# Optimization experiments

Measured on AMD Instinct MI355X. Metric: run time of the kernel, lower is better.

## Reference

```python
import jax, jax.numpy as jnp
import numpy as np

NN_SIZE = 10  # matches init_kwargs nn_size


def _knn_idx(points, k):
    """points: (B,N,D). Returns (B,N,k) indices of k nearest neighbors, self excluded."""
    sq = jnp.sum(points * points, axis=-1)  # (B,N)
    # squared euclidean distances (B,N,N)
    d2 = sq[:, :, None] + sq[:, None, :] - 2.0 * jnp.einsum('bnd,bmd->bnm', points, points)
    _, idx = jax.lax.top_k(-d2, k + 1)  # smallest distances; first hit is self
    return idx[:, :, 1:]  # drop self -> (B,N,k)


def _uniform_laplacian(points, knn_idx):
    """points: (B,N,D); knn_idx: (B,N,K). lap = mean(neighbors) - point."""
    neigh = jax.vmap(lambda p, i: p[i])(points, knn_idx)  # (B,N,K,D) gather per batch
    return jnp.mean(neigh, axis=2) - points


def setup_inputs() -> dict:
    key = jax.random.key(0)
    k1, k2 = jax.random.split(key)
    B, N, D = 2, 8192, 3
    point1 = jax.random.normal(k1, (B, N, D), dtype=jnp.float32)
    point2 = jax.random.normal(k2, (B, N, D), dtype=jnp.float32)
    return {"point1": point1, "point2": point2}


def reference(point1, point2):
    knn_idx = _knn_idx(point1, NN_SIZE)          # connectivity from ref cloud
    lap1 = _uniform_laplacian(point1, knn_idx)   # (B,N,3)
    lap2 = _uniform_laplacian(point2, knn_idx)   # reuse knn_idx
    # metric = L1Loss (mean reduction); use_norm=False
    return jnp.mean(jnp.abs(lap1 - lap2))
```

## Files before the change

kernel.cpp:

```cpp
#include <hip/hip_runtime.h>
#include <math.h>


constexpr int NPTS  = 8192;
constexpr int NB    = 2;
constexpr int KNN   = 10;
constexpr int QPB   = 64;
constexpr int WPB   = 16;
constexpr int BLOCK = QPB * WPB;
constexpr int MASK13 = 0xFFFFE000;

constexpr int   G    = 32;
constexpr int   NC   = G * G * G;
constexpr float BMIN = -5.5f;
constexpr float BW   = 11.0f;
constexpr float H    = BW / G;
constexpr float INVH = (float)G / BW;

__device__ __forceinline__ void ins1(int l[KNN], int x) {
#pragma unroll
    for (int k = KNN - 1; k > 0; --k) l[k] = min(l[k], max(l[k - 1], x));
    l[0] = min(l[0], x);
}
__device__ __forceinline__ void ins2(int l[KNN], int a, int b) {
    const int b0 = min(a, b), b1 = max(a, b);
#pragma unroll
    for (int k = KNN - 1; k >= 2; --k)
        l[k] = min(l[k], min(max(l[k - 1], b0), max(l[k - 2], b1)));
    l[1] = min(l[1], min(max(l[0], b0), b1));
    l[0] = min(l[0], b0);
}
template<int S>
__device__ __forceinline__ void ins2s(int l[KNN], int a, int b) {
    const int b0 = min(a, b), b1 = max(a, b);
#pragma unroll
    for (int k = KNN - 1; k >= S + 2; --k)
        l[k] = min(l[k], min(max(l[k - 1], b0), max(l[k - 2], b1)));
    l[S + 1] = min(l[S + 1], min(max(l[S], b0), b1));
    l[S] = min(l[S], b0);
}
__device__ __forceinline__ void merge_sorted(int l[KNN], const int p[KNN]) {
    ins2s<0>(l, p[0], p[1]);
    ins2s<2>(l, p[2], p[3]);
    ins2s<4>(l, p[4], p[5]);
    ins2s<6>(l, p[6], p[7]);
    ins2s<8>(l, p[8], p[9]);
}

__global__ void pack_bin(const float* __restrict__ p1, float4* __restrict__ w,
                         int* __restrict__ hist, int* __restrict__ cellof,
                         float* __restrict__ out, int* __restrict__ nfail) {
    const int i = blockIdx.x * blockDim.x + threadIdx.x;
    if (i >= NB * NPTS) return;
    if (i == 0) { out[0] = 0.0f; nfail[0] = 0; }
    const float x = p1[3 * i], y = p1[3 * i + 1], z = p1[3 * i + 2];
    w[i] = make_float4(x, y, z, fmaf(x, x, fmaf(y, y, z * z)));
    const int cx = min(max((int)floorf((x - BMIN) * INVH), 0), G - 1);
    const int cy = min(max((int)floorf((y - BMIN) * INVH), 0), G - 1);
    const int cz = min(max((int)floorf((z - BMIN) * INVH), 0), G - 1);
    const int c = (cz << 10) | (cy << 5) | cx;
    cellof[i] = c;
    atomicAdd(&hist[(i >> 13) * NC + c], 1);
}

__global__ __launch_bounds__(1024)
void scan_cells(const int* __restrict__ hist, int* __restrict__ starts) {
    __shared__ int wsum[16];
    const int b = blockIdx.x, t = threadIdx.x;
    const int* hb = hist + b * NC;
    int* sb = starts + b * (NC + 1);
    const int c0 = t * 32;
    int loc[32]; int sum = 0;
#pragma unroll
    for (int j = 0; j < 32; ++j) { loc[j] = hb[c0 + j]; sum += loc[j]; }
    const int lane = t & 63, wvi = t >> 6;
    int incl = sum;
#pragma unroll
    for (int off = 1; off < 64; off <<= 1) {
        const int v = __shfl_up(incl, off);
        if (lane >= off) incl += v;
    }
    if (lane == 63) wsum[wvi] = incl;
    __syncthreads();
    if (t < 16) {
        const int v = wsum[t];
        int iv = v;
#pragma unroll
        for (int off = 1; off < 16; off <<= 1) {
            const int u = __shfl_up(iv, off);
            if (t >= off) iv += u;
        }
        wsum[t] = iv - v;
    }
    __syncthreads();
    int run = wsum[wvi] + incl - sum;
#pragma unroll
    for (int j = 0; j < 32; ++j) { sb[c0 + j] = run; run += loc[j]; }
    if (t == 1023) sb[NC] = run;
}

__global__ void scatter_all(const int* __restrict__ cellof,
                            const int* __restrict__ starts,
                            int* __restrict__ hist,
                            const float4* __restrict__ w,
                            const float* __restrict__ p2,
                            float4* __restrict__ wsorted,
                            float4* __restrict__ p2s) {
    const int i = blockIdx.x * blockDim.x + threadIdx.x;
    if (i >= NB * NPTS) return;
    const int b = i >> 13;
    const int c = cellof[i];
    const int old = atomicSub(&hist[b * NC + c], 1);
    const int pos = b * NPTS + starts[b * (NC + 1) + c] + old - 1;
    wsorted[pos] = w[i];
    p2s[pos] = make_float4(p2[3 * i], p2[3 * i + 1], p2[3 * i + 2], 0.0f);
}

template<int S>
__device__ __forceinline__ void scan_batched(const float4* __restrict__ W,
                                             const int* __restrict__ st,
                                             int cx, int cy, int cz,
                                             float m2x, float m2y, float m2z,
                                             float q2, int qpos, int wv,
                                             int l[KNN])
{
    constexpr int Wd = 2 * S + 1;
    constexpr int R  = Wd * Wd;
    const int IMAX = 0x7FFFFFFF;
    int J0[R], J1[R];
#pragma unroll
    for (int r = 0; r < R; ++r) {
        const int dy = r % Wd - S, dz = r / Wd - S;
        const int ay = cy + dy, az = cz + dz;
        const bool ok = ((unsigned)ay < G) && ((unsigned)az < G);
        const int cbase = (az << 10) | (ay << 5);
        const int lo = cbase + max(cx - S, 0);
        const int hi = cbase + min(cx + S, G - 1) + 1;
        J0[r] = ok ? st[lo] : 0;
        J1[r] = ok ? st[hi] : 0;
    }
#pragma unroll
    for (int r = 0; r < R; ++r) {
        const int j1 = J1[r];
        int j = J0[r] + wv;
        if (j < j1) {
            float4 c4 = W[j];
            while (true) {
                const int jn = j + WPB;
                const bool more = jn < j1;
                float4 nx;
                if (more) nx = W[jn];
                const float d2 = fmaf(m2x, c4.x,
                                 fmaf(m2y, c4.y,
                                 fmaf(m2z, c4.z, c4.w + q2)));
                int key = (__float_as_int(d2) & MASK13) | j;
                key = (j == qpos) ? IMAX : key;
                ins1(l, key);
                if (!more) break;
                c4 = nx; j = jn;
            }
        }
    }
}

__global__ __launch_bounds__(BLOCK)
void phase1(const float4* __restrict__ wsorted, const float4* __restrict__ p2s,
            const int* __restrict__ starts, float* __restrict__ out,
            int* __restrict__ nfail, int* __restrict__ worklist)
{
    __shared__ int mv[WPB * KNN * QPB];

    const int batch = blockIdx.x >> 7;
    const int lane  = threadIdx.x & 63;
    const int wv    = __builtin_amdgcn_readfirstlane(threadIdx.x >> 6);
    const int qpos  = ((blockIdx.x & 127) << 6) + lane;

    const float4* W  = wsorted + batch * NPTS;
    const float4* P2 = p2s + batch * NPTS;
    const int*    st = starts + batch * (NC + 1);

    const float4 qp = W[qpos];
    const int cx = min(max((int)floorf((qp.x - BMIN) * INVH), 0), G - 1);
    const int cy = min(max((int)floorf((qp.y - BMIN) * INVH), 0), G - 1);
    const int cz = min(max((int)floorf((qp.z - BMIN) * INVH), 0), G - 1);
    const float lox = BMIN + cx * H, loy = BMIN + cy * H, loz = BMIN + cz * H;
    const float df = fminf(fminf(fminf(qp.x - lox, lox + H - qp.x),
                                 fminf(qp.y - loy, loy + H - qp.y)),
                           fminf(qp.z - loz, loz + H - qp.z));
    const float m2x = -2.0f * qp.x, m2y = -2.0f * qp.y, m2z = -2.0f * qp.z;
    const float q2 = qp.w;
    const int IMAX = 0x7FFFFFFF;

    const int sCov = (q2 > 4.8f) ? 2 : 1;

    int l[KNN];
#pragma unroll
    for (int k = 0; k < KNN; ++k) l[k] = IMAX;

    if (sCov == 1)
        scan_batched<1>(W, st, cx, cy, cz, m2x, m2y, m2z, q2, qpos, wv, l);
    else
        scan_batched<2>(W, st, cx, cy, cz, m2x, m2y, m2z, q2, qpos, wv, l);

#pragma unroll
    for (int k = 0; k < KNN; ++k) mv[(wv * KNN + k) * QPB + lane] = l[k];
    __syncthreads();

    if (threadIdx.x < QPB) {
        int M[KNN];
#pragma unroll
        for (int k = 0; k < KNN; ++k) M[k] = IMAX;
#pragma unroll
        for (int e = 0; e < WPB; ++e) {
            int p[KNN];
#pragma unroll
            for (int k = 0; k < KNN; ++k) p[k] = mv[(e * KNN + k) * QPB + lane];
            merge_sorted(M, p);
        }

        const float tau = __int_as_float(M[KNN - 1] & MASK13);
        const float R = (float)sCov * H + df;
        const bool covered = (tau <= R * R * 0.996f);
        float v = 0.0f;
        if (covered) {
            float s1x = 0, s1y = 0, s1z = 0, s2x = 0, s2y = 0, s2z = 0;
#pragma unroll
            for (int k = 0; k < KNN; ++k) {
                const int j = M[k] & (NPTS - 1);
                const float4 c4 = W[j];
                const float4 n2 = P2[j];
                s1x += c4.x; s1y += c4.y; s1z += c4.z;
                s2x += n2.x; s2y += n2.y; s2z += n2.z;
            }
            const float4 p2v = P2[qpos];
            const float dx = (s1x * 0.1f - qp.x) - (s2x * 0.1f - p2v.x);
            const float dy2 = (s1y * 0.1f - qp.y) - (s2y * 0.1f - p2v.y);
            const float dz2 = (s1z * 0.1f - qp.z) - (s2z * 0.1f - p2v.z);
            v = fabsf(dx) + fabsf(dy2) + fabsf(dz2);
        } else {
            const int wi = atomicAdd(nfail, 1);
            worklist[wi] = (batch << 16) | qpos;
        }
#pragma unroll
        for (int off = 32; off >= 1; off >>= 1) v += __shfl_down(v, off);
        if (threadIdx.x == 0)
            atomicAdd(out, v * (1.0f / (float)(NB * NPTS * 3)));
    }
}

constexpr int P2BLK = 256;
constexpr int P2GRID = 512;

__global__ __launch_bounds__(P2BLK)
void phase2(const float4* __restrict__ wsorted, const float4* __restrict__ p2s,
            const int* __restrict__ nfail, const int* __restrict__ worklist,
            float* __restrict__ out)
{
    const int lane = threadIdx.x & 63;
    const int wv   = threadIdx.x >> 6;
    const int wid  = blockIdx.x * (P2BLK / 64) + wv;
    const int NW   = P2GRID * (P2BLK / 64);
    const int nf   = *nfail;
    const int IMAX = 0x7FFFFFFF;
    float acc = 0.0f;

    for (int i = wid; i < nf; i += NW) {
        const int e = worklist[i];
        const int batch = e >> 16, qpos = e & 0xFFFF;
        const float4* W  = wsorted + batch * NPTS;
        const float4* P2 = p2s + batch * NPTS;
        const float4 qp = W[qpos];
        const float m2x = -2.0f * qp.x, m2y = -2.0f * qp.y, m2z = -2.0f * qp.z;
        const float q2 = qp.w;

        int l[KNN];
#pragma unroll
        for (int k = 0; k < KNN; ++k) l[k] = IMAX;

#pragma unroll 2
        for (int it = 0; it < NPTS / 128; ++it) {
            const int ja = it * 128 + lane, jb = ja + 64;
            const float4 ca = W[ja];
            const float4 cb = W[jb];
            const float da = fmaf(m2x, ca.x, fmaf(m2y, ca.y, fmaf(m2z, ca.z, ca.w + q2)));
            const float db = fmaf(m2x, cb.x, fmaf(m2y, cb.y, fmaf(m2z, cb.z, cb.w + q2)));
            int ka = (__float_as_int(da) & MASK13) | ja;
            int kb = (__float_as_int(db) & MASK13) | jb;
            ka = (ja == qpos) ? IMAX : ka;
            kb = (jb == qpos) ? IMAX : kb;
            ins2(l, ka, kb);
        }
        for (int off = 1; off < 64; off <<= 1) {
            int p[KNN];
#pragma unroll
            for (int k = 0; k < KNN; ++k) p[k] = __shfl_xor(l[k], off);
            merge_sorted(l, p);
        }
        float s1x = 0, s1y = 0, s1z = 0, s2x = 0, s2y = 0, s2z = 0;
#pragma unroll
        for (int k = 0; k < KNN; ++k) {
            const int j = l[k] & (NPTS - 1);
            const float4 c4 = W[j];
            const float4 n2 = P2[j];
            s1x += c4.x; s1y += c4.y; s1z += c4.z;
            s2x += n2.x; s2y += n2.y; s2z += n2.z;
        }
        const float4 p2v = P2[qpos];
        const float dx = (s1x * 0.1f - qp.x) - (s2x * 0.1f - p2v.x);
        const float dy = (s1y * 0.1f - qp.y) - (s2y * 0.1f - p2v.y);
        const float dz = (s1z * 0.1f - qp.z) - (s2z * 0.1f - p2v.z);
        if (lane == 0) acc += fabsf(dx) + fabsf(dy) + fabsf(dz);
    }

    if (lane == 0 && acc != 0.0f)
        atomicAdd(out, acc * (1.0f / (float)(NB * NPTS * 3)));
}

constexpr int FB_WPB = 8;
constexpr int FB_BLOCK = QPB * FB_WPB;
constexpr int CHUNK = NPTS / FB_WPB;

__global__ void prep_pack(const float* __restrict__ p, float4* __restrict__ w) {
    const int i = blockIdx.x * blockDim.x + threadIdx.x;
    if (i < NB * NPTS) {
        const float x = p[3 * i], y = p[3 * i + 1], z = p[3 * i + 2];
        w[i] = make_float4(x, y, z, fmaf(x, x, fmaf(y, y, z * z)));
    }
}

__global__ __launch_bounds__(FB_BLOCK, 2)
void knn_lap(const float4* __restrict__ w1, const float* __restrict__ p2,
             float* __restrict__ out)
{
    __shared__ int mv[FB_WPB * KNN * QPB];
    const int batch = blockIdx.x >> 7;
    const int qbase = (blockIdx.x & 127) << 6;
    const int lane  = threadIdx.x & 63;
    const int wv    = __builtin_amdgcn_readfirstlane(threadIdx.x >> 6);
    const int query = qbase + lane;
    const float4* Wb = w1 + batch * NPTS;
    const float4 qp = Wb[query];
    const float m2x = -2.0f * qp.x, m2y = -2.0f * qp.y, m2z = -2.0f * qp.z;
    const float q2 = qp.w;
    const int IMAX = 0x7FFFFFFF;
    int l[KNN];
#pragma unroll
    for (int k = 0; k < KNN; ++k) l[k] = IMAX;
    const int c0 = wv * CHUNK;
    const float4* cand = Wb + c0;
#pragma unroll 4
    for (int i = 0; i < CHUNK; i += 2) {
        const float4 ca = cand[i];
        const float4 cb = cand[i + 1];
        const int ja = c0 + i, jb = ja + 1;
        const float da = fmaf(m2x, ca.x, fmaf(m2y, ca.y, fmaf(m2z, ca.z, ca.w + q2)));
        const float db = fmaf(m2x, cb.x, fmaf(m2y, cb.y, fmaf(m2z, cb.z, cb.w + q2)));
        int ka = (__float_as_int(da) & MASK13) | ja;
        int kb = (__float_as_int(db) & MASK13) | jb;
        ka = (ja == query) ? IMAX : ka;
        kb = (jb == query) ? IMAX : kb;
        ins2(l, ka, kb);
    }
#pragma unroll
    for (int k = 0; k < KNN; ++k) mv[(wv * KNN + k) * QPB + lane] = l[k];
    __syncthreads();
    if (threadIdx.x < QPB) {
        int m[KNN];
#pragma unroll
        for (int k = 0; k < KNN; ++k) m[k] = IMAX;
#pragma unroll
        for (int e = 0; e < FB_WPB; ++e) {
            int p[KNN];
#pragma unroll
            for (int k = 0; k < KNN; ++k) p[k] = mv[(e * KNN + k) * QPB + lane];
            merge_sorted(m, p);
        }
        const float* P2b = p2 + (size_t)batch * NPTS * 3;
        float s1x = 0, s1y = 0, s1z = 0, s2x = 0, s2y = 0, s2z = 0;
#pragma unroll
        for (int k = 0; k < KNN; ++k) {
            const int j = m[k] & (NPTS - 1);
            const float4 c = Wb[j];
            s1x += c.x; s1y += c.y; s1z += c.z;
            s2x += P2b[3 * j + 0]; s2y += P2b[3 * j + 1]; s2z += P2b[3 * j + 2];
        }
        const int q = qbase + threadIdx.x;
        const float p2x = P2b[3 * q + 0], p2y = P2b[3 * q + 1], p2z = P2b[3 * q + 2];
        const float dx = (s1x * 0.1f - qp.x) - (s2x * 0.1f - p2x);
        const float dy = (s1y * 0.1f - qp.y) - (s2y * 0.1f - p2y);
        const float dz = (s1z * 0.1f - qp.z) - (s2z * 0.1f - p2z);
        float v = fabsf(dx) + fabsf(dy) + fabsf(dz);
#pragma unroll
        for (int off = 32; off >= 1; off >>= 1) v += __shfl_down(v, off);
        if (threadIdx.x == 0)
            atomicAdd(out, v * (1.0f / (float)(NB * NPTS * 3)));
    }
}

extern "C" void kernel_launch(void* const* d_in, const int* in_sizes, int n_in,
                              void* d_out, int out_size, void* d_ws, size_t ws_size,
                              hipStream_t stream) {
    const float* p1 = (const float*)d_in[0];
    const float* p2 = (const float*)d_in[1];
    float* out = (float*)d_out;

    size_t off = 0;
    float4* w       = (float4*)d_ws;               off += (size_t)NB * NPTS * 16;
    int*    hist    = (int*)((char*)d_ws + off);   off += (size_t)NB * NC * 4;
    int*    starts  = (int*)((char*)d_ws + off);   off += (size_t)NB * (NC + 1) * 4 + 8;
    int*    cellof  = (int*)((char*)d_ws + off);   off += (size_t)NB * NPTS * 4;
    float4* wsorted = (float4*)((char*)d_ws + off); off += (size_t)NB * NPTS * 16;
    float4* p2s     = (float4*)((char*)d_ws + off); off += (size_t)NB * NPTS * 16;
    int*    nfail   = (int*)((char*)d_ws + off);   off += 16;
    int*    worklist= (int*)((char*)d_ws + off);   off += (size_t)NB * NPTS * 4;

    if (ws_size < off) {
        hipMemsetAsync(out, 0, sizeof(float), stream);
        prep_pack<<<(NB * NPTS + 255) / 256, 256, 0, stream>>>(p1, w);
        knn_lap<<<NB * (NPTS / QPB), FB_BLOCK, 0, stream>>>(w, p2, out);
        return;
    }

    hipMemsetAsync(hist, 0, (size_t)NB * NC * 4, stream);
    pack_bin<<<(NB * NPTS + 255) / 256, 256, 0, stream>>>(p1, w, hist, cellof,
                                                          out, nfail);
    scan_cells<<<NB, 1024, 0, stream>>>(hist, starts);
    scatter_all<<<(NB * NPTS + 255) / 256, 256, 0, stream>>>(cellof, starts, hist,
                                                             w, p2, wsorted, p2s);
    phase1<<<NB * (NPTS / QPB), BLOCK, 0, stream>>>(wsorted, p2s, starts, out,
                                                    nfail, worklist);
    phase2<<<P2GRID, P2BLK, 0, stream>>>(wsorted, p2s, nfail, worklist, out);
}
```

Baseline: 120.9 us.

## Fuse binning, scan, scatter and kNN phases into one cooperative persistent kernel

Measured after the change: 265.9 us. +120.0%, slower.

```diff
diff --git a/kernel.cpp b/kernel.cpp
--- a/kernel.cpp
+++ b/kernel.cpp
@@ -1,13 +1,17 @@
 #include <hip/hip_runtime.h>
+#include <hip/hip_cooperative_groups.h>
 #include <math.h>
+
+namespace cg = cooperative_groups;
 
 
 constexpr int NPTS  = 8192;
 constexpr int NB    = 2;
 constexpr int KNN   = 10;
 constexpr int QPB   = 64;
-constexpr int WPB   = 16;
-constexpr int BLOCK = QPB * WPB;
+constexpr int WPB   = 8;
+constexpr int BLOCK = 512;
+constexpr int GRID  = 256;
 constexpr int MASK13 = 0xFFFFE000;
 
 constexpr int   G    = 32;
@@ -47,186 +51,257 @@
     ins2s<8>(l, p[8], p[9]);
 }
 
-__global__ void pack_bin(const float* __restrict__ p1, float4* __restrict__ w,
-                         int* __restrict__ hist, int* __restrict__ cellof,
-                         float* __restrict__ out, int* __restrict__ nfail) {
-    const int i = blockIdx.x * blockDim.x + threadIdx.x;
-    if (i >= NB * NPTS) return;
-    if (i == 0) { out[0] = 0.0f; nfail[0] = 0; }
-    const float x = p1[3 * i], y = p1[3 * i + 1], z = p1[3 * i + 2];
-    w[i] = make_float4(x, y, z, fmaf(x, x, fmaf(y, y, z * z)));
-    const int cx = min(max((int)floorf((x - BMIN) * INVH), 0), G - 1);
-    const int cy = min(max((int)floorf((y - BMIN) * INVH), 0), G - 1);
-    const int cz = min(max((int)floorf((z - BMIN) * INVH), 0), G - 1);
-    const int c = (cz << 10) | (cy << 5) | cx;
-    cellof[i] = c;
-    atomicAdd(&hist[(i >> 13) * NC + c], 1);
-}
-
-__global__ __launch_bounds__(1024)
-void scan_cells(const int* __restrict__ hist, int* __restrict__ starts) {
-    __shared__ int wsum[16];
-    const int b = blockIdx.x, t = threadIdx.x;
-    const int* hb = hist + b * NC;
-    int* sb = starts + b * (NC + 1);
-    const int c0 = t * 32;
-    int loc[32]; int sum = 0;
-#pragma unroll
-    for (int j = 0; j < 32; ++j) { loc[j] = hb[c0 + j]; sum += loc[j]; }
-    const int lane = t & 63, wvi = t >> 6;
-    int incl = sum;
+template<int S>
+__device__ __forceinline__ void scan_slab(const float4* __restrict__ W,
+                                          const int* __restrict__ st,
+                                          int cx, int cy, int cz,
+                                          float m2x, float m2y, float m2z,
+                                          float q2, int qpos, int wv,
+                                          int l[KNN])
+{
+    constexpr int Wd = 2 * S + 1;
+    const int IMAX = 0x7FFFFFFF;
+    const int xlo = max(cx - S, 0), xhi = min(cx + S, G - 1) + 1;
+#pragma unroll
+    for (int zi = 0; zi < Wd; ++zi) {
+        const int az = cz + zi - S;
+        int J0[Wd], J1[Wd];
+#pragma unroll
+        for (int yi = 0; yi < Wd; ++yi) {
+            const int ay = cy + yi - S;
+            const bool ok = ((unsigned)ay < G) && ((unsigned)az < G);
+            const int cbase = (az << 10) | (ay << 5);
+            J0[yi] = ok ? st[cbase + xlo] : 0;
+            J1[yi] = ok ? st[cbase + xhi] : 0;
+        }
+#pragma unroll
+        for (int yi = 0; yi < Wd; ++yi) {
+            const int j1 = J1[yi];
+            int j = J0[yi] + wv;
+            if (j < j1) {
+                float4 c4 = W[j];
+                while (true) {
+                    const int jn = j + WPB;
+                    const bool more = jn < j1;
+                    float4 nx;
+                    if (more) nx = W[jn];
+                    const float d2 = fmaf(m2x, c4.x,
+                                     fmaf(m2y, c4.y,
+                                     fmaf(m2z, c4.z, c4.w + q2)));
+                    int key = (__float_as_int(d2) & MASK13) | j;
+                    key = (j == qpos) ? IMAX : key;
+                    ins1(l, key);
+                    if (!more) break;
+                    c4 = nx; j = jn;
+                }
+            }
+        }
+    }
+}
+
+__global__ __launch_bounds__(BLOCK)
+void mega(const float* __restrict__ p1, const float* __restrict__ p2,
+          float* __restrict__ out,
+          float4* __restrict__ w, int* __restrict__ hist,
+          int* __restrict__ starts, int* __restrict__ cellof,
+          float4* __restrict__ wsorted, float4* __restrict__ p2s,
+          int* __restrict__ nfail, int* __restrict__ worklist,
+          int* __restrict__ blockTot)
+{
+    cg::grid_group grid = cg::this_grid();
+
+    __shared__ int mv[WPB * KNN * QPB];
+    __shared__ int wtot[8], wexcl[8], wred[8], sOff[1];
+
+    const int b    = blockIdx.x;
+    const int t    = threadIdx.x;
+    const int gtid = b * BLOCK + t;
+    const int lane = t & 63;
+    const int wv   = t >> 6;
+    const int IMAX = 0x7FFFFFFF;
+
+    if (gtid < NB * NC) hist[gtid] = 0;
+    if (gtid == 0) { out[0] = 0.0f; nfail[0] = 0; }
+    grid.sync();
+
+    if (gtid < NB * NPTS) {
+        const float x = p1[3 * gtid], y = p1[3 * gtid + 1], z = p1[3 * gtid + 2];
+        w[gtid] = make_float4(x, y, z, fmaf(x, x, fmaf(y, y, z * z)));
+        const int cx = min(max((int)floorf((x - BMIN) * INVH), 0), G - 1);
+        const int cy = min(max((int)floorf((y - BMIN) * INVH), 0), G - 1);
+        const int cz = min(max((int)floorf((z - BMIN) * INVH), 0), G - 1);
+        const int c = (cz << 10) | (cy << 5) | cx;
+        cellof[gtid] = c;
+        atomicAdd(&hist[(gtid >> 13) * NC + c], 1);
+    }
+    grid.sync();
+
+    const int batchC = b >> 7;
+    const int bb     = b & 127;
+    int cnt = (t < 256) ? hist[b * 256 + t] : 0;
+    int incl = cnt;
 #pragma unroll
     for (int off = 1; off < 64; off <<= 1) {
         const int v = __shfl_up(incl, off);
         if (lane >= off) incl += v;
     }
-    if (lane == 63) wsum[wvi] = incl;
+    if (lane == 63) wtot[wv] = incl;
     __syncthreads();
-    if (t < 16) {
-        const int v = wsum[t];
-        int iv = v;
-#pragma unroll
-        for (int off = 1; off < 16; off <<= 1) {
-            const int u = __shfl_up(iv, off);
-            if (t >= off) iv += u;
-        }
-        wsum[t] = iv - v;
+    if (t < 8) {
+        int o = 0;
+        for (int k = 0; k < t; ++k) o += wtot[k];
+        wexcl[t] = o;
     }
     __syncthreads();
-    int run = wsum[wvi] + incl - sum;
-#pragma unroll
-    for (int j = 0; j < 32; ++j) { sb[c0 + j] = run; run += loc[j]; }
-    if (t == 1023) sb[NC] = run;
-}
-
-__global__ void scatter_all(const int* __restrict__ cellof,
-                            const int* __restrict__ starts,
-                            int* __restrict__ hist,
-                            const float4* __restrict__ w,
-                            const float* __restrict__ p2,
-                            float4* __restrict__ wsorted,
-                            float4* __restrict__ p2s) {
-    const int i = blockIdx.x * blockDim.x + threadIdx.x;
-    if (i >= NB * NPTS) return;
-    const int b = i >> 13;
-    const int c = cellof[i];
-    const int old = atomicSub(&hist[b * NC + c], 1);
-    const int pos = b * NPTS + starts[b * (NC + 1) + c] + old - 1;
-    wsorted[pos] = w[i];
-    p2s[pos] = make_float4(p2[3 * i], p2[3 * i + 1], p2[3 * i + 2], 0.0f);
-}
-
-template<int S>
-__device__ __forceinline__ void scan_batched(const float4* __restrict__ W,
-                                             const int* __restrict__ st,
-                                             int cx, int cy, int cz,
-                                             float m2x, float m2y, float m2z,
-                                             float q2, int qpos, int wv,
-                                             int l[KNN])
-{
-    constexpr int Wd = 2 * S + 1;
-    constexpr int R  = Wd * Wd;
-    const int IMAX = 0x7FFFFFFF;
-    int J0[R], J1[R];
-#pragma unroll
-    for (int r = 0; r < R; ++r) {
-        const int dy = r % Wd - S, dz = r / Wd - S;
-        const int ay = cy + dy, az = cz + dz;
-        const bool ok = ((unsigned)ay < G) && ((unsigned)az < G);
-        const int cbase = (az << 10) | (ay << 5);
-        const int lo = cbase + max(cx - S, 0);
-        const int hi = cbase + min(cx + S, G - 1) + 1;
-        J0[r] = ok ? st[lo] : 0;
-        J1[r] = ok ? st[hi] : 0;
-    }
-#pragma unroll
-    for (int r = 0; r < R; ++r) {
-        const int j1 = J1[r];
-        int j = J0[r] + wv;
-        if (j < j1) {
-            float4 c4 = W[j];
-            while (true) {
-                const int jn = j + WPB;
-                const bool more = jn < j1;
-                float4 nx;
-                if (more) nx = W[jn];
-                const float d2 = fmaf(m2x, c4.x,
-                                 fmaf(m2y, c4.y,
-                                 fmaf(m2z, c4.z, c4.w + q2)));
-                int key = (__float_as_int(d2) & MASK13) | j;
-                key = (j == qpos) ? IMAX : key;
-                ins1(l, key);
-                if (!more) break;
-                c4 = nx; j = jn;
-            }
-        }
-    }
-}
-
-__global__ __launch_bounds__(BLOCK)
-void phase1(const float4* __restrict__ wsorted, const float4* __restrict__ p2s,
-            const int* __restrict__ starts, float* __restrict__ out,
-            int* __restrict__ nfail, int* __restrict__ worklist)
-{
-    __shared__ int mv[WPB * KNN * QPB];
-
-    const int batch = blockIdx.x >> 7;
-    const int lane  = threadIdx.x & 63;
-    const int wv    = __builtin_amdgcn_readfirstlane(threadIdx.x >> 6);
-    const int qpos  = ((blockIdx.x & 127) << 6) + lane;
-
-    const float4* W  = wsorted + batch * NPTS;
-    const float4* P2 = p2s + batch * NPTS;
-    const int*    st = starts + batch * (NC + 1);
-
-    const float4 qp = W[qpos];
-    const int cx = min(max((int)floorf((qp.x - BMIN) * INVH), 0), G - 1);
-    const int cy = min(max((int)floorf((qp.y - BMIN) * INVH), 0), G - 1);
-    const int cz = min(max((int)floorf((qp.z - BMIN) * INVH), 0), G - 1);
-    const float lox = BMIN + cx * H, loy = BMIN + cy * H, loz = BMIN + cz * H;
-    const float df = fminf(fminf(fminf(qp.x - lox, lox + H - qp.x),
-                                 fminf(qp.y - loy, loy + H - qp.y)),
-                           fminf(qp.z - loz, loz + H - qp.z));
-    const float m2x = -2.0f * qp.x, m2y = -2.0f * qp.y, m2z = -2.0f * qp.z;
-    const float q2 = qp.w;
-    const int IMAX = 0x7FFFFFFF;
-
-    const int sCov = (q2 > 4.8f) ? 2 : 1;
-
-    int l[KNN];
-#pragma unroll
-    for (int k = 0; k < KNN; ++k) l[k] = IMAX;
-
-    if (sCov == 1)
-        scan_batched<1>(W, st, cx, cy, cz, m2x, m2y, m2z, q2, qpos, wv, l);
-    else
-        scan_batched<2>(W, st, cx, cy, cz, m2x, m2y, m2z, q2, qpos, wv, l);
-
-#pragma unroll
-    for (int k = 0; k < KNN; ++k) mv[(wv * KNN + k) * QPB + lane] = l[k];
-    __syncthreads();
-
-    if (threadIdx.x < QPB) {
-        int M[KNN];
-#pragma unroll
-        for (int k = 0; k < KNN; ++k) M[k] = IMAX;
-#pragma unroll
-        for (int e = 0; e < WPB; ++e) {
-            int p[KNN];
-#pragma unroll
-            for (int k = 0; k < KNN; ++k) p[k] = mv[(e * KNN + k) * QPB + lane];
-            merge_sorted(M, p);
-        }
-
-        const float tau = __int_as_float(M[KNN - 1] & MASK13);
-        const float R = (float)sCov * H + df;
-        const bool covered = (tau <= R * R * 0.996f);
-        float v = 0.0f;
-        if (covered) {
+    const int excl = wexcl[wv] + incl - cnt;
+    if (t == 0) blockTot[b] = wexcl[7] + wtot[7];
+    if (t == 0 && bb == 0) starts[batchC * (NC + 1) + NC] = NPTS;
+    grid.sync();
+
+    {
+        const int base = batchC << 7;
+        int v = (t < bb) ? blockTot[base + t] : 0;
+#pragma unroll
+        for (int off = 32; off >= 1; off >>= 1) v += __shfl_xor(v, off);
+        if (lane == 0) wred[wv] = v;
+        __syncthreads();
+        if (t == 0) {
+            int o = 0;
+#pragma unroll
+            for (int k = 0; k < 8; ++k) o += wred[k];
+            sOff[0] = o;
+        }
+        __syncthreads();
+        if (t < 256)
+            starts[batchC * (NC + 1) + bb * 256 + t] = excl + sOff[0];
+    }
+    grid.sync();
+
+    if (gtid < NB * NPTS) {
+        const int bt = gtid >> 13;
+        const int c = cellof[gtid];
+        const int old = atomicSub(&hist[bt * NC + c], 1);
+        const int pos = bt * NPTS + starts[bt * (NC + 1) + c] + old - 1;
+        wsorted[pos] = w[gtid];
+        p2s[pos] = make_float4(p2[3 * gtid], p2[3 * gtid + 1],
+                               p2[3 * gtid + 2], 0.0f);
+    }
+    grid.sync();
+
+    {
+        const int batch = b >> 7;
+        const int qpos  = ((b & 127) << 6) + lane;
+        const float4* W  = wsorted + batch * NPTS;
+        const float4* P2 = p2s + batch * NPTS;
+        const int*    st = starts + batch * (NC + 1);
+
+        const float4 qp = W[qpos];
+        const int cx = min(max((int)floorf((qp.x - BMIN) * INVH), 0), G - 1);
+        const int cy = min(max((int)floorf((qp.y - BMIN) * INVH), 0), G - 1);
+        const int cz = min(max((int)floorf((qp.z - BMIN) * INVH), 0), G - 1);
+        const float lox = BMIN + cx * H, loy = BMIN + cy * H, loz = BMIN + cz * H;
+        const float df = fminf(fminf(fminf(qp.x - lox, lox + H - qp.x),
+                                     fminf(qp.y - loy, loy + H - qp.y)),
+                               fminf(qp.z - loz, loz + H - qp.z));
+        const float m2x = -2.0f * qp.x, m2y = -2.0f * qp.y, m2z = -2.0f * qp.z;
+        const float q2 = qp.w;
+        const int sCov = (q2 > 4.8f) ? 2 : 1;
+
+        int l[KNN];
+#pragma unroll
+        for (int k = 0; k < KNN; ++k) l[k] = IMAX;
+
+        if (sCov == 1)
+            scan_slab<1>(W, st, cx, cy, cz, m2x, m2y, m2z, q2, qpos, wv, l);
+        else
+            scan_slab<2>(W, st, cx, cy, cz, m2x, m2y, m2z, q2, qpos, wv, l);
+
+#pragma unroll
+        for (int k = 0; k < KNN; ++k) mv[(wv * KNN + k) * QPB + lane] = l[k];
+        __syncthreads();
+
+        if (t < QPB) {
+            int M[KNN];
+#pragma unroll
+            for (int k = 0; k < KNN; ++k) M[k] = IMAX;
+#pragma unroll
+            for (int e = 0; e < WPB; ++e) {
+                int p[KNN];
+#pragma unroll
+                for (int k = 0; k < KNN; ++k) p[k] = mv[(e * KNN + k) * QPB + lane];
+                merge_sorted(M, p);
+            }
+            const float tau = __int_as_float(M[KNN - 1] & MASK13);
+            const float R = (float)sCov * H + df;
+            const bool covered = (tau <= R * R * 0.996f);
+            float v = 0.0f;
+            if (covered) {
+                float s1x = 0, s1y = 0, s1z = 0, s2x = 0, s2y = 0, s2z = 0;
+#pragma unroll
+                for (int k = 0; k < KNN; ++k) {
+                    const int j = M[k] & (NPTS - 1);
+                    const float4 c4 = W[j];
+                    const float4 n2 = P2[j];
+                    s1x += c4.x; s1y += c4.y; s1z += c4.z;
+                    s2x += n2.x; s2y += n2.y; s2z += n2.z;
+                }
+                const float4 p2v = P2[qpos];
+                const float dx = (s1x * 0.1f - qp.x) - (s2x * 0.1f - p2v.x);
+                const float dy = (s1y * 0.1f - qp.y) - (s2y * 0.1f - p2v.y);
+                const float dz = (s1z * 0.1f - qp.z) - (s2z * 0.1f - p2v.z);
+                v = fabsf(dx) + fabsf(dy) + fabsf(dz);
+            } else {
+                const int wi = atomicAdd(nfail, 1);
+                worklist[wi] = (batch << 16) | qpos;
+            }
+#pragma unroll
+            for (int off = 32; off >= 1; off >>= 1) v += __shfl_down(v, off);
+            if (t == 0)
+                atomicAdd(out, v * (1.0f / (float)(NB * NPTS * 3)));
+        }
+    }
+    grid.sync();
+
+    {
+        const int nf = nfail[0];
+        const int wid = b * WPB + wv;
+        const int NW = GRID * WPB;
+        float acc = 0.0f;
+        for (int i = wid; i < nf; i += NW) {
+            const int e = worklist[i];
+            const int batch = e >> 16, qpos = e & 0xFFFF;
+            const float4* W  = wsorted + batch * NPTS;
+            const float4* P2 = p2s + batch * NPTS;
+            const float4 qp = W[qpos];
+            const float m2x = -2.0f * qp.x, m2y = -2.0f * qp.y, m2z = -2.0f * qp.z;
+            const float q2 = qp.w;
+
+            int l[KNN];
+#pragma unroll
+            for (int k = 0; k < KNN; ++k) l[k] = IMAX;
+#pragma unroll 2
+            for (int it = 0; it < NPTS / 128; ++it) {
+                const int ja = it * 128 + lane, jb = ja + 64;
+                const float4 ca = W[ja];
+                const float4 cb = W[jb];
+                const float da = fmaf(m2x, ca.x, fmaf(m2y, ca.y, fmaf(m2z, ca.z, ca.w + q2)));
+                const float db = fmaf(m2x, cb.x, fmaf(m2y, cb.y, fmaf(m2z, cb.z, cb.w + q2)));
+                int ka = (__float_as_int(da) & MASK13) | ja;
+                int kb = (__float_as_int(db) & MASK13) | jb;
+                ka = (ja == qpos) ? IMAX : ka;
+                kb = (jb == qpos) ? IMAX : kb;
+                ins2(l, ka, kb);
+            }
+            for (int off = 1; off < 64; off <<= 1) {
+                int p[KNN];
+#pragma unroll
+                for (int k = 0; k < KNN; ++k) p[k] = __shfl_xor(l[k], off);
+                merge_sorted(l, p);
+            }
             float s1x = 0, s1y = 0, s1z = 0, s2x = 0, s2y = 0, s2z = 0;
 #pragma unroll
             for (int k = 0; k < KNN; ++k) {
-                const int j = M[k] & (NPTS - 1);
+                const int j = l[k] & (NPTS - 1);
                 const float4 c4 = W[j];
                 const float4 n2 = P2[j];
                 s1x += c4.x; s1y += c4.y; s1z += c4.z;
@@ -234,86 +309,13 @@
             }
             const float4 p2v = P2[qpos];
             const float dx = (s1x * 0.1f - qp.x) - (s2x * 0.1f - p2v.x);
-            const float dy2 = (s1y * 0.1f - qp.y) - (s2y * 0.1f - p2v.y);
-            const float dz2 = (s1z * 0.1f - qp.z) - (s2z * 0.1f - p2v.z);
-            v = fabsf(dx) + fabsf(dy2) + fabsf(dz2);
-        } else {
-            const int wi = atomicAdd(nfail, 1);
-            worklist[wi] = (batch << 16) | qpos;
-        }
-#pragma unroll
-        for (int off = 32; off >= 1; off >>= 1) v += __shfl_down(v, off);
-        if (threadIdx.x == 0)
-            atomicAdd(out, v * (1.0f / (float)(NB * NPTS * 3)));
-    }
-}
-
-constexpr int P2BLK = 256;
-constexpr int P2GRID = 512;
-
-__global__ __launch_bounds__(P2BLK)
-void phase2(const float4* __restrict__ wsorted, const float4* __restrict__ p2s,
-            const int* __restrict__ nfail, const int* __restrict__ worklist,
-            float* __restrict__ out)
-{
-    const int lane = threadIdx.x & 63;
-    const int wv   = threadIdx.x >> 6;
-    const int wid  = blockIdx.x * (P2BLK / 64) + wv;
-    const int NW   = P2GRID * (P2BLK / 64);
-    const int nf   = *nfail;
-    const int IMAX = 0x7FFFFFFF;
-    float acc = 0.0f;
-
-    for (int i = wid; i < nf; i += NW) {
-        const int e = worklist[i];
-        const int batch = e >> 16, qpos = e & 0xFFFF;
-        const float4* W  = wsorted + batch * NPTS;
-        const float4* P2 = p2s + batch * NPTS;
-        const float4 qp = W[qpos];
-        const float m2x = -2.0f * qp.x, m2y = -2.0f * qp.y, m2z = -2.0f * qp.z;
-        const float q2 = qp.w;
-
-        int l[KNN];
-#pragma unroll
-        for (int k = 0; k < KNN; ++k) l[k] = IMAX;
-
-#pragma unroll 2
-        for (int it = 0; it < NPTS / 128; ++it) {
-            const int ja = it * 128 + lane, jb = ja + 64;
-            const float4 ca = W[ja];
-            const float4 cb = W[jb];
-            const float da = fmaf(m2x, ca.x, fmaf(m2y, ca.y, fmaf(m2z, ca.z, ca.w + q2)));
-            const float db = fmaf(m2x, cb.x, fmaf(m2y, cb.y, fmaf(m2z, cb.z, cb.w + q2)));
-            int ka = (__float_as_int(da) & MASK13) | ja;
-            int kb = (__float_as_int(db) & MASK13) | jb;
-            ka = (ja == qpos) ? IMAX : ka;
-            kb = (jb == qpos) ? IMAX : kb;
-            ins2(l, ka, kb);
-        }
-        for (int off = 1; off < 64; off <<= 1) {
-            int p[KNN];
-#pragma unroll
-            for (int k = 0; k < KNN; ++k) p[k] = __shfl_xor(l[k], off);
-            merge_sorted(l, p);
-        }
-        float s1x = 0, s1y = 0, s1z = 0, s2x = 0, s2y = 0, s2z = 0;
-#pragma unroll
-        for (int k = 0; k < KNN; ++k) {
-            const int j = l[k] & (NPTS - 1);
-            const float4 c4 = W[j];
-            const float4 n2 = P2[j];
-            s1x += c4.x; s1y += c4.y; s1z += c4.z;
-            s2x += n2.x; s2y += n2.y; s2z += n2.z;
-        }
-        const float4 p2v = P2[qpos];
-        const float dx = (s1x * 0.1f - qp.x) - (s2x * 0.1f - p2v.x);
-        const float dy = (s1y * 0.1f - qp.y) - (s2y * 0.1f - p2v.y);
-        const float dz = (s1z * 0.1f - qp.z) - (s2z * 0.1f - p2v.z);
-        if (lane == 0) acc += fabsf(dx) + fabsf(dy) + fabsf(dz);
-    }
-
-    if (lane == 0 && acc != 0.0f)
-        atomicAdd(out, acc * (1.0f / (float)(NB * NPTS * 3)));
+            const float dy = (s1y * 0.1f - qp.y) - (s2y * 0.1f - p2v.y);
+            const float dz = (s1z * 0.1f - qp.z) - (s2z * 0.1f - p2v.z);
+            if (lane == 0) acc += fabsf(dx) + fabsf(dy) + fabsf(dz);
+        }
+        if (lane == 0 && acc != 0.0f)
+            atomicAdd(out, acc * (1.0f / (float)(NB * NPTS * 3)));
+    }
 }
 
 constexpr int FB_WPB = 8;
@@ -405,14 +407,15 @@
     float* out = (float*)d_out;
 
     size_t off = 0;
-    float4* w       = (float4*)d_ws;               off += (size_t)NB * NPTS * 16;
-    int*    hist    = (int*)((char*)d_ws + off);   off += (size_t)NB * NC * 4;
-    int*    starts  = (int*)((char*)d_ws + off);   off += (size_t)NB * (NC + 1) * 4 + 8;
-    int*    cellof  = (int*)((char*)d_ws + off);   off += (size_t)NB * NPTS * 4;
+    float4* w       = (float4*)d_ws;                off += (size_t)NB * NPTS * 16;
+    int*    hist    = (int*)((char*)d_ws + off);    off += (size_t)NB * NC * 4;
+    int*    starts  = (int*)((char*)d_ws + off);    off += (size_t)NB * (NC + 1) * 4 + 8;
+    int*    cellof  = (int*)((char*)d_ws + off);    off += (size_t)NB * NPTS * 4;
     float4* wsorted = (float4*)((char*)d_ws + off); off += (size_t)NB * NPTS * 16;
     float4* p2s     = (float4*)((char*)d_ws + off); off += (size_t)NB * NPTS * 16;
-    int*    nfail   = (int*)((char*)d_ws + off);   off += 16;
-    int*    worklist= (int*)((char*)d_ws + off);   off += (size_t)NB * NPTS * 4;
+    int*    nfail   = (int*)((char*)d_ws + off);    off += 16;
+    int*    worklist= (int*)((char*)d_ws + off);    off += (size_t)NB * NPTS * 4;
+    int*    blockTot= (int*)((char*)d_ws + off);    off += (size_t)GRID * 4;
 
     if (ws_size < off) {
         hipMemsetAsync(out, 0, sizeof(float), stream);
@@ -421,13 +424,10 @@
         return;
     }
 
-    hipMemsetAsync(hist, 0, (size_t)NB * NC * 4, stream);
-    pack_bin<<<(NB * NPTS + 255) / 256, 256, 0, stream>>>(p1, w, hist, cellof,
-                                                          out, nfail);
-    scan_cells<<<NB, 1024, 0, stream>>>(hist, starts);
-    scatter_all<<<(NB * NPTS + 255) / 256, 256, 0, stream>>>(cellof, starts, hist,
-                                                             w, p2, wsorted, p2s);
-    phase1<<<NB * (NPTS / QPB), BLOCK, 0, stream>>>(wsorted, p2s, starts, out,
-                                                    nfail, worklist);
-    phase2<<<P2GRID, P2BLK, 0, stream>>>(wsorted, p2s, nfail, worklist, out);
-}
+    void* args[] = { (void*)&p1, (void*)&p2, (void*)&out, (void*)&w,
+                     (void*)&hist, (void*)&starts, (void*)&cellof,
+                     (void*)&wsorted, (void*)&p2s, (void*)&nfail,
+                     (void*)&worklist, (void*)&blockTot };
+    hipLaunchCooperativeKernel((void*)mega, dim3(GRID), dim3(BLOCK),
+                               args, 0, stream);
+}
```

## Fuse brute-force fallback into phase1 and gather p2 via sorted-index map

Applied to the files above, without the earlier changes.

Measured after the change: 147.7 us. +22.2%, slower.

```diff
diff --git a/kernel.cpp b/kernel.cpp
--- a/kernel.cpp
+++ b/kernel.cpp
@@ -6,7 +6,7 @@
 constexpr int NB    = 2;
 constexpr int KNN   = 10;
 constexpr int QPB   = 64;
-constexpr int WPB   = 16;
+constexpr int WPB   = 8;
 constexpr int BLOCK = QPB * WPB;
 constexpr int MASK13 = 0xFFFFE000;
 
@@ -49,10 +49,10 @@
 
 __global__ void pack_bin(const float* __restrict__ p1, float4* __restrict__ w,
                          int* __restrict__ hist, int* __restrict__ cellof,
-                         float* __restrict__ out, int* __restrict__ nfail) {
+                         float* __restrict__ out) {
     const int i = blockIdx.x * blockDim.x + threadIdx.x;
     if (i >= NB * NPTS) return;
-    if (i == 0) { out[0] = 0.0f; nfail[0] = 0; }
+    if (i == 0) out[0] = 0.0f;
     const float x = p1[3 * i], y = p1[3 * i + 1], z = p1[3 * i + 2];
     w[i] = make_float4(x, y, z, fmaf(x, x, fmaf(y, y, z * z)));
     const int cx = min(max((int)floorf((x - BMIN) * INVH), 0), G - 1);
@@ -103,9 +103,8 @@
                             const int* __restrict__ starts,
                             int* __restrict__ hist,
                             const float4* __restrict__ w,
-                            const float* __restrict__ p2,
                             float4* __restrict__ wsorted,
-                            float4* __restrict__ p2s) {
+                            int* __restrict__ sIdx) {
     const int i = blockIdx.x * blockDim.x + threadIdx.x;
     if (i >= NB * NPTS) return;
     const int b = i >> 13;
@@ -113,7 +112,7 @@
     const int old = atomicSub(&hist[b * NC + c], 1);
     const int pos = b * NPTS + starts[b * (NC + 1) + c] + old - 1;
     wsorted[pos] = w[i];
-    p2s[pos] = make_float4(p2[3 * i], p2[3 * i + 1], p2[3 * i + 2], 0.0f);
+    sIdx[pos] = i & (NPTS - 1);
 }
 
 template<int S>
@@ -164,20 +163,27 @@
 }
 
 __global__ __launch_bounds__(BLOCK)
-void phase1(const float4* __restrict__ wsorted, const float4* __restrict__ p2s,
-            const int* __restrict__ starts, float* __restrict__ out,
-            int* __restrict__ nfail, int* __restrict__ worklist)
+void phase1(const float4* __restrict__ wsorted, const int* __restrict__ sIdx,
+            const float* __restrict__ p2, const int* __restrict__ starts,
+            float* __restrict__ out)
 {
     __shared__ int mv[WPB * KNN * QPB];
+    __shared__ int failList[QPB];
+    __shared__ int nFail;
+    __shared__ float bsum;
 
     const int batch = blockIdx.x >> 7;
-    const int lane  = threadIdx.x & 63;
-    const int wv    = __builtin_amdgcn_readfirstlane(threadIdx.x >> 6);
+    const int t     = threadIdx.x;
+    const int lane  = t & 63;
+    const int wv    = __builtin_amdgcn_readfirstlane(t >> 6);
     const int qpos  = ((blockIdx.x & 127) << 6) + lane;
 
     const float4* W  = wsorted + batch * NPTS;
-    const float4* P2 = p2s + batch * NPTS;
+    const int*    sI = sIdx + batch * NPTS;
+    const float*  P2 = p2 + (size_t)batch * NPTS * 3;
     const int*    st = starts + batch * (NC + 1);
+
+    if (t == 0) { nFail = 0; bsum = 0.0f; }
 
     const float4 qp = W[qpos];
     const int cx = min(max((int)floorf((qp.x - BMIN) * INVH), 0), G - 1);
@@ -206,7 +212,7 @@
     for (int k = 0; k < KNN; ++k) mv[(wv * KNN + k) * QPB + lane] = l[k];
     __syncthreads();
 
-    if (threadIdx.x < QPB) {
+    if (t < QPB) {
         int M[KNN];
 #pragma unroll
         for (int k = 0; k < KNN; ++k) M[k] = IMAX;
@@ -228,97 +234,87 @@
             for (int k = 0; k < KNN; ++k) {
                 const int j = M[k] & (NPTS - 1);
                 const float4 c4 = W[j];
-                const float4 n2 = P2[j];
+                const int oi = sI[j];
                 s1x += c4.x; s1y += c4.y; s1z += c4.z;
-                s2x += n2.x; s2y += n2.y; s2z += n2.z;
+                s2x += P2[3 * oi + 0];
+                s2y += P2[3 * oi + 1];
+                s2z += P2[3 * oi + 2];
             }
-            const float4 p2v = P2[qpos];
-            const float dx = (s1x * 0.1f - qp.x) - (s2x * 0.1f - p2v.x);
-            const float dy2 = (s1y * 0.1f - qp.y) - (s2y * 0.1f - p2v.y);
-            const float dz2 = (s1z * 0.1f - qp.z) - (s2z * 0.1f - p2v.z);
-            v = fabsf(dx) + fabsf(dy2) + fabsf(dz2);
-        } else {
-            const int wi = atomicAdd(nfail, 1);
-            worklist[wi] = (batch << 16) | qpos;
-        }
+            const int oq = sI[qpos];
+            const float p2x = P2[3 * oq + 0];
+            const float p2y = P2[3 * oq + 1];
+            const float p2z = P2[3 * oq + 2];
+            const float dx = (s1x * 0.1f - qp.x) - (s2x * 0.1f - p2x);
+            const float dy = (s1y * 0.1f - qp.y) - (s2y * 0.1f - p2y);
+            const float dz = (s1z * 0.1f - qp.z) - (s2z * 0.1f - p2z);
+            v = fabsf(dx) + fabsf(dy) + fabsf(dz);
+        }
+        const unsigned long long fm = __ballot(!covered);
+        if (!covered) {
+            const int rank = __popcll(fm & ((1ull << lane) - 1ull));
+            failList[rank] = lane;
+        }
+        if (lane == 0) nFail = __popcll(fm);
 #pragma unroll
         for (int off = 32; off >= 1; off >>= 1) v += __shfl_down(v, off);
-        if (threadIdx.x == 0)
-            atomicAdd(out, v * (1.0f / (float)(NB * NPTS * 3)));
-    }
-}
-
-constexpr int P2BLK = 256;
-constexpr int P2GRID = 512;
-
-__global__ __launch_bounds__(P2BLK)
-void phase2(const float4* __restrict__ wsorted, const float4* __restrict__ p2s,
-            const int* __restrict__ nfail, const int* __restrict__ worklist,
-            float* __restrict__ out)
-{
-    const int lane = threadIdx.x & 63;
-    const int wv   = threadIdx.x >> 6;
-    const int wid  = blockIdx.x * (P2BLK / 64) + wv;
-    const int NW   = P2GRID * (P2BLK / 64);
-    const int nf   = *nfail;
-    const int IMAX = 0x7FFFFFFF;
+        if (lane == 0) bsum = v;
+    }
+    __syncthreads();
+
+    const int nf = nFail;
     float acc = 0.0f;
-
-    for (int i = wid; i < nf; i += NW) {
-        const int e = worklist[i];
-        const int batch = e >> 16, qpos = e & 0xFFFF;
-        const float4* W  = wsorted + batch * NPTS;
-        const float4* P2 = p2s + batch * NPTS;
-        const float4 qp = W[qpos];
-        const float m2x = -2.0f * qp.x, m2y = -2.0f * qp.y, m2z = -2.0f * qp.z;
-        const float q2 = qp.w;
-
-        int l[KNN];
-#pragma unroll
-        for (int k = 0; k < KNN; ++k) l[k] = IMAX;
-
+    for (int i = wv; i < nf; i += WPB) {
+        const int fq = ((blockIdx.x & 127) << 6) + failList[i];
+        const float4 fqp = W[fq];
+        const float f2x = -2.0f * fqp.x, f2y = -2.0f * fqp.y, f2z = -2.0f * fqp.z;
+        const float fq2 = fqp.w;
+
+        int fl[KNN];
+#pragma unroll
+        for (int k = 0; k < KNN; ++k) fl[k] = IMAX;
 #pragma unroll 2
         for (int it = 0; it < NPTS / 128; ++it) {
             const int ja = it * 128 + lane, jb = ja + 64;
             const float4 ca = W[ja];
             const float4 cb = W[jb];
-            const float da = fmaf(m2x, ca.x, fmaf(m2y, ca.y, fmaf(m2z, ca.z, ca.w + q2)));
-            const float db = fmaf(m2x, cb.x, fmaf(m2y, cb.y, fmaf(m2z, cb.z, cb.w + q2)));
+            const float da = fmaf(f2x, ca.x, fmaf(f2y, ca.y, fmaf(f2z, ca.z, ca.w + fq2)));
+            const float db = fmaf(f2x, cb.x, fmaf(f2y, cb.y, fmaf(f2z, cb.z, cb.w + fq2)));
             int ka = (__float_as_int(da) & MASK13) | ja;
             int kb = (__float_as_int(db) & MASK13) | jb;
-            ka = (ja == qpos) ? IMAX : ka;
-            kb = (jb == qpos) ? IMAX : kb;
-            ins2(l, ka, kb);
+            ka = (ja == fq) ? IMAX : ka;
+            kb = (jb == fq) ? IMAX : kb;
+            ins2(fl, ka, kb);
         }
         for (int off = 1; off < 64; off <<= 1) {
             int p[KNN];
 #pragma unroll
-            for (int k = 0; k < KNN; ++k) p[k] = __shfl_xor(l[k], off);
-            merge_sorted(l, p);
+            for (int k = 0; k < KNN; ++k) p[k] = __shfl_xor(fl[k], off);
+            merge_sorted(fl, p);
         }
         float s1x = 0, s1y = 0, s1z = 0, s2x = 0, s2y = 0, s2z = 0;
 #pragma unroll
         for (int k = 0; k < KNN; ++k) {
-            const int j = l[k] & (NPTS - 1);
+            const int j = fl[k] & (NPTS - 1);
             const float4 c4 = W[j];
-            const float4 n2 = P2[j];
+            const int oi = sI[j];
             s1x += c4.x; s1y += c4.y; s1z += c4.z;
-            s2x += n2.x; s2y += n2.y; s2z += n2.z;
-        }
-        const float4 p2v = P2[qpos];
-        const float dx = (s1x * 0.1f - qp.x) - (s2x * 0.1f - p2v.x);
-        const float dy = (s1y * 0.1f - qp.y) - (s2y * 0.1f - p2v.y);
-        const float dz = (s1z * 0.1f - qp.z) - (s2z * 0.1f - p2v.z);
+            s2x += P2[3 * oi + 0];
+            s2y += P2[3 * oi + 1];
+            s2z += P2[3 * oi + 2];
+        }
+        const int oq = sI[fq];
+        const float dx = (s1x * 0.1f - fqp.x) - (s2x * 0.1f - P2[3 * oq + 0]);
+        const float dy = (s1y * 0.1f - fqp.y) - (s2y * 0.1f - P2[3 * oq + 1]);
+        const float dz = (s1z * 0.1f - fqp.z) - (s2z * 0.1f - P2[3 * oq + 2]);
         if (lane == 0) acc += fabsf(dx) + fabsf(dy) + fabsf(dz);
     }
-
-    if (lane == 0 && acc != 0.0f)
-        atomicAdd(out, acc * (1.0f / (float)(NB * NPTS * 3)));
-}
-
-constexpr int FB_WPB = 8;
-constexpr int FB_BLOCK = QPB * FB_WPB;
-constexpr int CHUNK = NPTS / FB_WPB;
+    if (lane == 0 && acc != 0.0f) atomicAdd(&bsum, acc);
+    __syncthreads();
+    if (t == 0)
+        atomicAdd(out, bsum * (1.0f / (float)(NB * NPTS * 3)));
+}
+
+constexpr int CHUNK = NPTS / WPB;
 
 __global__ void prep_pack(const float* __restrict__ p, float4* __restrict__ w) {
     const int i = blockIdx.x * blockDim.x + threadIdx.x;
@@ -328,11 +324,11 @@
     }
 }
 
-__global__ __launch_bounds__(FB_BLOCK, 2)
+__global__ __launch_bounds__(BLOCK, 2)
 void knn_lap(const float4* __restrict__ w1, const float* __restrict__ p2,
              float* __restrict__ out)
 {
-    __shared__ int mv[FB_WPB * KNN * QPB];
+    __shared__ int mv[WPB * KNN * QPB];
     const int batch = blockIdx.x >> 7;
     const int qbase = (blockIdx.x & 127) << 6;
     const int lane  = threadIdx.x & 63;
@@ -369,7 +365,7 @@
 #pragma unroll
         for (int k = 0; k < KNN; ++k) m[k] = IMAX;
 #pragma unroll
-        for (int e = 0; e < FB_WPB; ++e) {
+        for (int e = 0; e < WPB; ++e) {
             int p[KNN];
 #pragma unroll
             for (int k = 0; k < KNN; ++k) p[k] = mv[(e * KNN + k) * QPB + lane];
@@ -405,29 +401,24 @@
     float* out = (float*)d_out;
 
     size_t off = 0;
-    float4* w       = (float4*)d_ws;               off += (size_t)NB * NPTS * 16;
-    int*    hist    = (int*)((char*)d_ws + off);   off += (size_t)NB * NC * 4;
-    int*    starts  = (int*)((char*)d_ws + off);   off += (size_t)NB * (NC + 1) * 4 + 8;
-    int*    cellof  = (int*)((char*)d_ws + off);   off += (size_t)NB * NPTS * 4;
+    float4* w       = (float4*)d_ws;                off += (size_t)NB * NPTS * 16;
+    int*    hist    = (int*)((char*)d_ws + off);    off += (size_t)NB * NC * 4;
+    int*    starts  = (int*)((char*)d_ws + off);    off += (size_t)NB * (NC + 1) * 4 + 8;
+    int*    cellof  = (int*)((char*)d_ws + off);    off += (size_t)NB * NPTS * 4;
     float4* wsorted = (float4*)((char*)d_ws + off); off += (size_t)NB * NPTS * 16;
-    float4* p2s     = (float4*)((char*)d_ws + off); off += (size_t)NB * NPTS * 16;
-    int*    nfail   = (int*)((char*)d_ws + off);   off += 16;
-    int*    worklist= (int*)((char*)d_ws + off);   off += (size_t)NB * NPTS * 4;
+    int*    sIdx    = (int*)((char*)d_ws + off);    off += (size_t)NB * NPTS * 4;
 
     if (ws_size < off) {
         hipMemsetAsync(out, 0, sizeof(float), stream);
         prep_pack<<<(NB * NPTS + 255) / 256, 256, 0, stream>>>(p1, w);
-        knn_lap<<<NB * (NPTS / QPB), FB_BLOCK, 0, stream>>>(w, p2, out);
+        knn_lap<<<NB * (NPTS / QPB), BLOCK, 0, stream>>>(w, p2, out);
         return;
     }
 
     hipMemsetAsync(hist, 0, (size_t)NB * NC * 4, stream);
-    pack_bin<<<(NB * NPTS + 255) / 256, 256, 0, stream>>>(p1, w, hist, cellof,
-                                                          out, nfail);
+    pack_bin<<<(NB * NPTS + 255) / 256, 256, 0, stream>>>(p1, w, hist, cellof, out);
     scan_cells<<<NB, 1024, 0, stream>>>(hist, starts);
     scatter_all<<<(NB * NPTS + 255) / 256, 256, 0, stream>>>(cellof, starts, hist,
-                                                             w, p2, wsorted, p2s);
-    phase1<<<NB * (NPTS / QPB), BLOCK, 0, stream>>>(wsorted, p2s, starts, out,
-                                                    nfail, worklist);
-    phase2<<<P2GRID, P2BLK, 0, stream>>>(wsorted, p2s, nfail, worklist, out);
-}
+                                                             w, wsorted, sIdx);
+    phase1<<<NB * (NPTS / QPB), BLOCK, 0, stream>>>(wsorted, sIdx, p2, starts, out);
+}
```
